# Optimization experiments

Hardware: AMD Instinct MI355X
Metric: run time of the kernel (lower is better)

Reference implementation:

```python
import jax, jax.numpy as jnp
import numpy as np

N_ITER = 5
EPS = 1e-20


def setup_inputs() -> dict:
    key = jax.random.key(0)
    k1, k2, k3 = jax.random.split(key, 3)
    M, J, I, K, N = 2, 2048, 2049, 8, 2
    X = jax.random.normal(k1, (M, J, I, 2), dtype=jnp.float32)
    # torch.rand(...) * (1 - 1e-8) + 1e-8  (hoisted out of forward for determinism)
    T0 = jax.random.uniform(k2, (I, K, N), dtype=jnp.float32) * (1 - 1e-8) + 1e-8
    V0 = jax.random.uniform(k3, (K, J, N), dtype=jnp.float32) * (1 - 1e-8) + 1e-8
    return {"X": X, "T0": T0, "V0": V0}


def _ilrma(X_ri, T0, V0):
    # X_ri: (M, J, I, 2) real -> Xc: (I, M, J) complex
    Xp = jnp.transpose(X_ri, (2, 0, 1, 3))
    Xc = jax.lax.complex(Xp[..., 0], Xp[..., 1])
    I_, M, J = Xc.shape
    N = T0.shape[2]
    W = jnp.broadcast_to(jnp.eye(N, M, dtype=Xc.dtype), (I_, N, M))  # (I, N, M)
    Y = jnp.einsum('inm,imj->inj', W, Xc)                            # (I, N, J)
    T, V = T0, V0
    invJ = jnp.asarray(1.0 / J, dtype=Xc.dtype)
    for _ in range(N_ITER):
        for n in range(N):
            Tn = T[:, :, n]            # (I, K)
            Vn = V[:, :, n]            # (K, J)
            Yn = Y[:, n, :]            # (I, J)
            # --- NMF multiplicative updates (vectorized over all I bins) ---
            Rn = Tn @ Vn                                        # (I, J)
            P = jnp.abs(Yn) ** 2 / (jnp.abs(Rn) ** 2 + EPS)     # |Y|^2 / R^2
            Rd = 1.0 / jnp.abs(Rn)                              # 1 / R
            Tn = Tn * jnp.sqrt((P @ Vn.T) / (Rd @ Vn.T))
            Rn = Tn @ Vn
            Vn = Vn * jnp.sqrt((Tn.T @ P) / (Tn.T @ Rd))
            Rn = Tn @ Vn                                        # updated source model
            T = T.at[:, :, n].set(Tn)
            V = V.at[:, :, n].set(Vn)
            # --- demixing vector update, batched over frequency bins I ---
            Xh = Xc / Rn[:, None, :]                            # (I, M, J)
            D = jnp.einsum('imj,ikj->imk', Xh, Xc) * invJ       # (I, M, M) (plain .T, no conj, as in source)
            WD = jnp.einsum('inm,imk->ink', W, D)               # (I, M, M)
            e = jnp.zeros((M,), dtype=Xc.dtype).at[n].set(1.0)
            rhs = jnp.broadcast_to(e[:, None], (I_, M, 1))
            b = jnp.linalg.solve(WD, rhs)[..., 0]               # (I, M)  == inv(W D) @ e_n
            nrm = jnp.einsum('im,imk,ik->i', b, D, b)           # b^T D b (complex, no conj)
            W = W.at[:, :, n].set(b / jnp.sqrt(nrm)[:, None])
        Y = jnp.einsum('inm,imj->inj', W, Xc)
    return Y


def reference(X, T0, V0):
    return _ilrma(X, T0, V0)
```

## Files before the change

### kernel.cpp

```cpp
#include <hip/hip_runtime.h>
#include <math.h>

#define I_  2049
#define M_  2
#define J_  2048
#define K_  8
#define N_  2
#define NITER 5
#define EPSF 1e-20f
#define INVJ (1.0/2048.0)
#define CHUNK 16
#define NCHUNK 129

__device__ float4 g_Xc[(size_t)I_*J_];
__device__ float2 g_T2[I_*K_];
__device__ float2 g_Told2[I_*K_];
__device__ float4 g_Vt4[(size_t)J_*4];
__device__ float2 g_W[I_*N_*M_];
__device__ float2 g_Wold[I_*N_*M_];
__device__ float2 g_pnum[(size_t)NCHUNK*K_*J_];
__device__ float2 g_pden[(size_t)NCHUNK*K_*J_];

__device__ __forceinline__ float frcp(float x) { return __builtin_amdgcn_rcpf(x); }

struct dcx { double x, y; };
__device__ __forceinline__ dcx cmul(dcx a, dcx b) { return {a.x*b.x - a.y*b.y, a.x*b.y + a.y*b.x}; }
__device__ __forceinline__ dcx cadd(dcx a, dcx b) { return {a.x + b.x, a.y + b.y}; }
__device__ __forceinline__ dcx csub(dcx a, dcx b) { return {a.x - b.x, a.y - b.y}; }
__device__ __forceinline__ dcx cneg(dcx a) { return {-a.x, -a.y}; }
__device__ __forceinline__ dcx cdiv(dcx a, dcx b) {
  double d = b.x*b.x + b.y*b.y;
  return {(a.x*b.x + a.y*b.y)/d, (a.y*b.x - a.x*b.y)/d};
}
__device__ __forceinline__ dcx csqrt_(dcx z) {
  double r = hypot(z.x, z.y);
  if (r == 0.0) return {0.0, 0.0};
  double t = sqrt(0.5*(r + fabs(z.x)));
  if (z.x >= 0.0) return {t, z.y/(2.0*t)};
  return {fabs(z.y)/(2.0*t), (z.y >= 0.0) ? t : -t};
}

__device__ __forceinline__ float2 cyn(float2 w0, float2 w1, float2 x0, float2 x1) {
  float2 y;
  y.x = w0.x*x0.x - w0.y*x0.y + w1.x*x1.x - w1.y*x1.y;
  y.y = w0.x*x0.y + w0.y*x0.x + w1.x*x1.y + w1.y*x1.x;
  return y;
}

__device__ __forceinline__ void solve12(int i, const double* s_, float2* wout) {
  dcx Wl[2][2];
  Wl[0][0] = {g_W[(size_t)i*4+0].x, g_W[(size_t)i*4+0].y};
  Wl[0][1] = {g_W[(size_t)i*4+1].x, g_W[(size_t)i*4+1].y};
  Wl[1][0] = {g_W[(size_t)i*4+2].x, g_W[(size_t)i*4+2].y};
  Wl[1][1] = {g_W[(size_t)i*4+3].x, g_W[(size_t)i*4+3].y};
#pragma unroll
  for (int n = 0; n < N_; n++) {
    dcx D00 = {s_[6*n+0]*INVJ, s_[6*n+1]*INVJ};
    dcx D01 = {s_[6*n+2]*INVJ, s_[6*n+3]*INVJ};
    dcx D11 = {s_[6*n+4]*INVJ, s_[6*n+5]*INVJ};
    dcx WD00 = cadd(cmul(Wl[0][0], D00), cmul(Wl[0][1], D01));
    dcx WD01 = cadd(cmul(Wl[0][0], D01), cmul(Wl[0][1], D11));
    dcx WD10 = cadd(cmul(Wl[1][0], D00), cmul(Wl[1][1], D01));
    dcx WD11 = cadd(cmul(Wl[1][0], D01), cmul(Wl[1][1], D11));
    dcx det = csub(cmul(WD00, WD11), cmul(WD01, WD10));
    dcx b0, b1;
    if (n == 0) { b0 = cdiv(WD11, det);        b1 = cdiv(cneg(WD10), det); }
    else        { b0 = cdiv(cneg(WD01), det);  b1 = cdiv(WD00, det); }
    dcx nrm = cadd(cmul(cmul(b0, b0), D00), cmul(cmul(b1, b1), D11));
    dcx tcr = cmul(cmul(b0, b1), D01); tcr.x *= 2.0; tcr.y *= 2.0;
    nrm = cadd(nrm, tcr);
    dcx sq = csqrt_(nrm);
    Wl[0][n] = cdiv(b0, sq);
    Wl[1][n] = cdiv(b1, sq);
  }
  float2 o00 = make_float2((float)Wl[0][0].x, (float)Wl[0][0].y);
  float2 o01 = make_float2((float)Wl[0][1].x, (float)Wl[0][1].y);
  float2 o10 = make_float2((float)Wl[1][0].x, (float)Wl[1][0].y);
  float2 o11 = make_float2((float)Wl[1][1].x, (float)Wl[1][1].y);
  g_W[(size_t)i*4+0] = o00; g_W[(size_t)i*4+1] = o01;
  g_W[(size_t)i*4+2] = o10; g_W[(size_t)i*4+3] = o11;
  g_Wold[(size_t)i*4+0] = o00; g_Wold[(size_t)i*4+1] = o01;
  g_Wold[(size_t)i*4+2] = o10; g_Wold[(size_t)i*4+3] = o11;
  wout[0] = o00; wout[1] = o01; wout[2] = o10; wout[3] = o11;
}

__global__ __launch_bounds__(256) void k_setup(const float* __restrict__ T0,
                                               const float* __restrict__ V0) {
  int idx = blockIdx.x*256 + threadIdx.x;
  if (idx < I_*K_) g_T2[idx] = ((const float2*)T0)[idx];
  if (idx < K_*J_) {
    int k = idx >> 11, j = idx & (J_-1);
    float2 v = ((const float2*)V0)[idx];
    float* vtf = (float*)g_Vt4;
    vtf[j*16 + k]     = v.x;
    vtf[j*16 + 8 + k] = v.y;
  }
  if (idx < I_*N_*M_) {
    int r = (idx >> 1) & 1, c = idx & 1;
    float2 v = make_float2((r == c) ? 1.f : 0.f, 0.f);
    g_W[idx] = v;
    g_Wold[idx] = v;
  }
}

__global__ __launch_bounds__(256) void k_transpose(const float* __restrict__ X) {
  __shared__ float2 s0[32][65];
  __shared__ float2 s1[32][65];
  int i0 = blockIdx.x*64, j0 = blockIdx.y*32;
  int lane = threadIdx.x & 63, row = threadIdx.x >> 6;
  const float2* X2 = (const float2*)X;
  int gi = i0 + lane;
  if (gi < I_) {
    for (int jj = row; jj < 32; jj += 4) {
      s0[jj][lane] = X2[(size_t)(0*J_ + j0 + jj)*I_ + gi];
      s1[jj][lane] = X2[(size_t)(1*J_ + j0 + jj)*I_ + gi];
    }
  }
  __syncthreads();
  int jj = threadIdx.x & 31, ii0 = threadIdx.x >> 5;
  for (int u = 0; u < 8; u++) {
    int ii = ii0*8 + u;
    int i = i0 + ii;
    if (i < I_) {
      float2 a = s0[jj][ii], b = s1[jj][ii];
      g_Xc[(size_t)i*J_ + j0 + jj] = make_float4(a.x, a.y, b.x, b.y);
    }
  }
}

__global__ __launch_bounds__(256) void k_tv(int doD) {
  int i = blockIdx.x, t = threadIdx.x;
  int wv = t >> 6, lane = t & 63;
  __shared__ float redD[4][12];
  __shared__ float2 sW[4];
  __shared__ float redT[4][32];

  float2 tk2[K_];
#pragma unroll
  for (int k = 0; k < K_; k++) tk2[k] = g_T2[(size_t)i*K_ + k];

  if (doD) {
    float4 xv[8];
#pragma unroll
    for (int s = 0; s < 8; s++) xv[s] = g_Xc[(size_t)i*J_ + wv*512 + s*64 + lane];
    float acc[12];
#pragma unroll
    for (int q = 0; q < 12; q++) acc[q] = 0.f;
#pragma unroll
    for (int s = 0; s < 8; s++) {
      int j = wv*512 + s*64 + lane;
      float4 vt0 = g_Vt4[(size_t)j*4+0], vt1 = g_Vt4[(size_t)j*4+1];
      float4 vt2 = g_Vt4[(size_t)j*4+2], vt3 = g_Vt4[(size_t)j*4+3];
      float vkx[K_] = {vt0.x,vt0.y,vt0.z,vt0.w,vt1.x,vt1.y,vt1.z,vt1.w};
      float vky[K_] = {vt2.x,vt2.y,vt2.z,vt2.w,vt3.x,vt3.y,vt3.z,vt3.w};
      float rn0 = 0.f, rn1 = 0.f;
#pragma unroll
      for (int k = 0; k < K_; k++) {
        rn0 = fmaf(tk2[k].x, vkx[k], rn0);
        rn1 = fmaf(tk2[k].y, vky[k], rn1);
      }
      float a0 = xv[s].x, b0 = xv[s].y, a1 = xv[s].z, b1 = xv[s].w;
      float d00r = a0*a0 - b0*b0, d00i = 2.f*a0*b0;
      float d01r = a0*a1 - b0*b1, d01i = a0*b1 + a1*b0;
      float d11r = a1*a1 - b1*b1, d11i = 2.f*a1*b1;
      float inv0 = frcp(rn0), inv1 = frcp(rn1);
      acc[0] = fmaf(d00r, inv0, acc[0]); acc[1] = fmaf(d00i, inv0, acc[1]);
      acc[2] = fmaf(d01r, inv0, acc[2]); acc[3] = fmaf(d01i, inv0, acc[3]);
      acc[4] = fmaf(d11r, inv0, acc[4]); acc[5] = fmaf(d11i, inv0, acc[5]);
      acc[6] = fmaf(d00r, inv1, acc[6]); acc[7] = fmaf(d00i, inv1, acc[7]);
      acc[8] = fmaf(d01r, inv1, acc[8]); acc[9] = fmaf(d01i, inv1, acc[9]);
      acc[10]= fmaf(d11r, inv1, acc[10]);acc[11]= fmaf(d11i, inv1, acc[11]);
    }
#pragma unroll
    for (int q = 0; q < 12; q++)
      for (int off = 32; off; off >>= 1) acc[q] += __shfl_down(acc[q], off);
    if (lane == 0) {
#pragma unroll
      for (int q = 0; q < 12; q++) redD[wv][q] = acc[q];
    }
    __syncthreads();
    if (t == 0) {
      double s_[12];
#pragma unroll
      for (int q = 0; q < 12; q++)
        s_[q] = (double)redD[0][q] + (double)redD[1][q] + (double)redD[2][q] + (double)redD[3][q];
      float2 w[4];
      solve12(i, s_, w);
      sW[0] = w[0]; sW[1] = w[1]; sW[2] = w[2]; sW[3] = w[3];
    }
  } else {
    if (t == 0) {
      sW[0] = g_Wold[(size_t)i*4+0]; sW[1] = g_Wold[(size_t)i*4+1];
      sW[2] = g_Wold[(size_t)i*4+2]; sW[3] = g_Wold[(size_t)i*4+3];
    }
  }
  __syncthreads();
  float2 w00 = sW[0], w01 = sW[1], w10 = sW[2], w11 = sW[3];

  float4 xv2[8];
#pragma unroll
  for (int s = 0; s < 8; s++) xv2[s] = g_Xc[(size_t)i*J_ + t + 256*s];
  float aN0[K_], aD0[K_], aN1[K_], aD1[K_];
#pragma unroll
  for (int k = 0; k < K_; k++) { aN0[k]=0.f; aD0[k]=0.f; aN1[k]=0.f; aD1[k]=0.f; }
#pragma unroll
  for (int s = 0; s < 8; s++) {
    int j = t + 256*s;
    float4 vt0 = g_Vt4[(size_t)j*4+0], vt1 = g_Vt4[(size_t)j*4+1];
    float4 vt2 = g_Vt4[(size_t)j*4+2], vt3 = g_Vt4[(size_t)j*4+3];
    float vkx[K_] = {vt0.x,vt0.y,vt0.z,vt0.w,vt1.x,vt1.y,vt1.z,vt1.w};
    float vky[K_] = {vt2.x,vt2.y,vt2.z,vt2.w,vt3.x,vt3.y,vt3.z,vt3.w};
    float rn0 = 0.f, rn1 = 0.f;
#pragma unroll
    for (int k = 0; k < K_; k++) {
      rn0 = fmaf(tk2[k].x, vkx[k], rn0);
      rn1 = fmaf(tk2[k].y, vky[k], rn1);
    }
    float2 x0 = make_float2(xv2[s].x, xv2[s].y);
    float2 x1 = make_float2(xv2[s].z, xv2[s].w);
    float2 y0 = cyn(w00, w01, x0, x1);
    float2 y1 = cyn(w10, w11, x0, x1);
    float p0  = (y0.x*y0.x + y0.y*y0.y) * frcp(rn0*rn0 + EPSF);
    float p1  = (y1.x*y1.x + y1.y*y1.y) * frcp(rn1*rn1 + EPSF);
    float rd0 = frcp(rn0), rd1 = frcp(rn1);
#pragma unroll
    for (int k = 0; k < K_; k++) {
      aN0[k] = fmaf(p0,  vkx[k], aN0[k]);
      aD0[k] = fmaf(rd0, vkx[k], aD0[k]);
      aN1[k] = fmaf(p1,  vky[k], aN1[k]);
      aD1[k] = fmaf(rd1, vky[k], aD1[k]);
    }
  }
#pragma unroll
  for (int k = 0; k < K_; k++)
    for (int off = 32; off; off >>= 1) {
      aN0[k] += __shfl_down(aN0[k], off);
      aD0[k] += __shfl_down(aD0[k], off);
      aN1[k] += __shfl_down(aN1[k], off);
      aD1[k] += __shfl_down(aD1[k], off);
    }
  if (lane == 0) {
#pragma unroll
    for (int k = 0; k < K_; k++) {
      redT[wv][k]      = aN0[k];
      redT[wv][8 + k]  = aD0[k];
      redT[wv][16 + k] = aN1[k];
      redT[wv][24 + k] = aD1[k];
    }
  }
  __syncthreads();
  if (t < 8) {
    int k = t;
    float n0 = redT[0][k]    + redT[1][k]    + redT[2][k]    + redT[3][k];
    float d0 = redT[0][8+k]  + redT[1][8+k]  + redT[2][8+k]  + redT[3][8+k];
    float n1 = redT[0][16+k] + redT[1][16+k] + redT[2][16+k] + redT[3][16+k];
    float d1 = redT[0][24+k] + redT[1][24+k] + redT[2][24+k] + redT[3][24+k];
    float2 tv = tk2[k];
    g_Told2[(size_t)i*K_ + k] = tv;
    g_T2[(size_t)i*K_ + k] = make_float2(tv.x * sqrtf(n0/d0), tv.y * sqrtf(n1/d1));
  }
}

__global__ __launch_bounds__(256) void k_vupd2() {
  int t  = threadIdx.x;
  int j  = blockIdx.x*256 + t;
  int c  = blockIdx.y;
  int i0 = c*CHUNK;
  int ni = I_ - i0; if (ni > CHUNK) ni = CHUNK;

  __shared__ float2 sWold[CHUNK*4];
  __shared__ float2 sTold[CHUNK*8];
  __shared__ float2 sT[CHUNK*8];
  for (int u = t; u < CHUNK*20; u += 256) {
    if (u < CHUNK*4) {
      int g = i0*4 + u;              if (g < I_*4) sWold[u] = g_Wold[g];
    } else if (u < CHUNK*12) {
      int g = i0*8 + (u - CHUNK*4);  if (g < I_*8) sTold[u - CHUNK*4] = g_Told2[g];
    } else {
      int g = i0*8 + (u - CHUNK*12); if (g < I_*8) sT[u - CHUNK*12] = g_T2[g];
    }
  }
  __syncthreads();

  float4 vt0 = g_Vt4[(size_t)j*4+0], vt1 = g_Vt4[(size_t)j*4+1];
  float4 vt2 = g_Vt4[(size_t)j*4+2], vt3 = g_Vt4[(size_t)j*4+3];
  float vkx[K_] = {vt0.x,vt0.y,vt0.z,vt0.w,vt1.x,vt1.y,vt1.z,vt1.w};
  float vky[K_] = {vt2.x,vt2.y,vt2.z,vt2.w,vt3.x,vt3.y,vt3.z,vt3.w};
  float aN0[K_], aD0[K_], aN1[K_], aD1[K_];
#pragma unroll
  for (int k = 0; k < K_; k++) { aN0[k]=0.f; aD0[k]=0.f; aN1[k]=0.f; aD1[k]=0.f; }

  auto body = [&](int ii, float4 xv) {
    float2 x0 = make_float2(xv.x, xv.y);
    float2 x1 = make_float2(xv.z, xv.w);
    float2 w00 = sWold[ii*4 + 0], w01 = sWold[ii*4 + 1];
    float2 w10 = sWold[ii*4 + 2], w11 = sWold[ii*4 + 3];
    float rn0 = 0.f, rn1 = 0.f;
#pragma unroll
    for (int k = 0; k < K_; k++) {
      float2 to = sTold[ii*8 + k];
      rn0 = fmaf(to.x, vkx[k], rn0);
      rn1 = fmaf(to.y, vky[k], rn1);
    }
    float2 y0 = cyn(w00, w01, x0, x1);
    float2 y1 = cyn(w10, w11, x0, x1);
    float p0  = (y0.x*y0.x + y0.y*y0.y) * frcp(rn0*rn0 + EPSF);
    float p1  = (y1.x*y1.x + y1.y*y1.y) * frcp(rn1*rn1 + EPSF);
    float rd0 = frcp(rn0), rd1 = frcp(rn1);
#pragma unroll
    for (int k = 0; k < K_; k++) {
      float2 tn = sT[ii*8 + k];
      aN0[k] = fmaf(tn.x, p0,  aN0[k]);
      aD0[k] = fmaf(tn.x, rd0, aD0[k]);
      aN1[k] = fmaf(tn.y, p1,  aN1[k]);
      aD1[k] = fmaf(tn.y, rd1, aD1[k]);
    }
  };

  int ii = 0;
  for (; ii + 8 <= ni; ii += 8) {
    float4 xv[8];
#pragma unroll
    for (int u = 0; u < 8; u++) xv[u] = g_Xc[(size_t)(i0 + ii + u)*J_ + j];
#pragma unroll
    for (int u = 0; u < 8; u++) body(ii + u, xv[u]);
  }
  for (; ii < ni; ii++) {
    float4 xv = g_Xc[(size_t)(i0 + ii)*J_ + j];
    body(ii, xv);
  }

  size_t base = (size_t)c*(K_*J_);
#pragma unroll
  for (int k = 0; k < K_; k++) {
    g_pnum[base + (size_t)k*J_ + j] = make_float2(aN0[k], aN1[k]);
    g_pden[base + (size_t)k*J_ + j] = make_float2(aD0[k], aD1[k]);
  }
}

__global__ __launch_bounds__(256) void k_vapply2() {
  int t = threadIdx.x;
  int idx = blockIdx.x*16 + (t & 15);
  int slice = t >> 4;
  int c0 = slice*9, c1 = c0 + 9; if (c1 > NCHUNK) c1 = NCHUNK;
  float2 sn = make_float2(0.f, 0.f), sd = make_float2(0.f, 0.f);
  for (int c = c0; c < c1; c++) {
    float2 a = g_pnum[(size_t)c*(K_*J_) + idx];
    float2 b = g_pden[(size_t)c*(K_*J_) + idx];
    sn.x += a.x; sn.y += a.y; sd.x += b.x; sd.y += b.y;
  }
  __shared__ float2 rN[16][16], rD[16][16];
  rN[slice][t & 15] = sn; rD[slice][t & 15] = sd;
  __syncthreads();
  if (t < 16) {
    float2 n = rN[0][t], d = rD[0][t];
#pragma unroll
    for (int s = 1; s < 16; s++) {
      n.x += rN[s][t].x; n.y += rN[s][t].y;
      d.x += rD[s][t].x; d.y += rD[s][t].y;
    }
    int kk = idx >> 11, j = idx & (J_-1);
    float* vtf = (float*)g_Vt4;
    float v0 = vtf[j*16 + kk], v1 = vtf[j*16 + 8 + kk];
    vtf[j*16 + kk]     = v0 * sqrtf(n.x/d.x);
    vtf[j*16 + 8 + kk] = v1 * sqrtf(n.y/d.y);
  }
}

__global__ __launch_bounds__(256) void k_yout(float* __restrict__ out, int cplx) {
  int i = blockIdx.x, t = threadIdx.x;
  int wv = t >> 6, lane = t & 63;
  __shared__ float redD[4][12];
  __shared__ float2 sW[4];

  float2 tk2[K_];
#pragma unroll
  for (int k = 0; k < K_; k++) tk2[k] = g_T2[(size_t)i*K_ + k];

  {
    float4 xv[8];
#pragma unroll
    for (int s = 0; s < 8; s++) xv[s] = g_Xc[(size_t)i*J_ + wv*512 + s*64 + lane];
    float acc[12];
#pragma unroll
    for (int q = 0; q < 12; q++) acc[q] = 0.f;
#pragma unroll
    for (int s = 0; s < 8; s++) {
      int j = wv*512 + s*64 + lane;
      float4 vt0 = g_Vt4[(size_t)j*4+0], vt1 = g_Vt4[(size_t)j*4+1];
      float4 vt2 = g_Vt4[(size_t)j*4+2], vt3 = g_Vt4[(size_t)j*4+3];
      float vkx[K_] = {vt0.x,vt0.y,vt0.z,vt0.w,vt1.x,vt1.y,vt1.z,vt1.w};
      float vky[K_] = {vt2.x,vt2.y,vt2.z,vt2.w,vt3.x,vt3.y,vt3.z,vt3.w};
      float rn0 = 0.f, rn1 = 0.f;
#pragma unroll
      for (int k = 0; k < K_; k++) {
        rn0 = fmaf(tk2[k].x, vkx[k], rn0);
        rn1 = fmaf(tk2[k].y, vky[k], rn1);
      }
      float a0 = xv[s].x, b0 = xv[s].y, a1 = xv[s].z, b1 = xv[s].w;
      float d00r = a0*a0 - b0*b0, d00i = 2.f*a0*b0;
      float d01r = a0*a1 - b0*b1, d01i = a0*b1 + a1*b0;
      float d11r = a1*a1 - b1*b1, d11i = 2.f*a1*b1;
      float inv0 = frcp(rn0), inv1 = frcp(rn1);
      acc[0] = fmaf(d00r, inv0, acc[0]); acc[1] = fmaf(d00i, inv0, acc[1]);
      acc[2] = fmaf(d01r, inv0, acc[2]); acc[3] = fmaf(d01i, inv0, acc[3]);
      acc[4] = fmaf(d11r, inv0, acc[4]); acc[5] = fmaf(d11i, inv0, acc[5]);
      acc[6] = fmaf(d00r, inv1, acc[6]); acc[7] = fmaf(d00i, inv1, acc[7]);
      acc[8] = fmaf(d01r, inv1, acc[8]); acc[9] = fmaf(d01i, inv1, acc[9]);
      acc[10]= fmaf(d11r, inv1, acc[10]);acc[11]= fmaf(d11i, inv1, acc[11]);
    }
#pragma unroll
    for (int q = 0; q < 12; q++)
      for (int off = 32; off; off >>= 1) acc[q] += __shfl_down(acc[q], off);
    if (lane == 0) {
#pragma unroll
      for (int q = 0; q < 12; q++) redD[wv][q] = acc[q];
    }
  }
  __syncthreads();
  if (t == 0) {
    double s_[12];
#pragma unroll
    for (int q = 0; q < 12; q++)
      s_[q] = (double)redD[0][q] + (double)redD[1][q] + (double)redD[2][q] + (double)redD[3][q];
    float2 w[4];
    solve12(i, s_, w);
    sW[0] = w[0]; sW[1] = w[1]; sW[2] = w[2]; sW[3] = w[3];
  }
  __syncthreads();
  float2 w00 = sW[0], w01 = sW[1], w10 = sW[2], w11 = sW[3];
  float2* out2 = (float2*)out;
#pragma unroll
  for (int s = 0; s < 8; s++) {
    int j = t + 256*s;
    float4 xv = g_Xc[(size_t)i*J_ + j];
    float2 x0 = make_float2(xv.x, xv.y);
    float2 x1 = make_float2(xv.z, xv.w);
    float2 y0 = cyn(w00, w01, x0, x1);
    float2 y1 = cyn(w10, w11, x0, x1);
    if (cplx) {
      out2[((size_t)i*N_ + 0)*J_ + j] = y0;
      out2[((size_t)i*N_ + 1)*J_ + j] = y1;
    } else {
      out[((size_t)i*N_ + 0)*J_ + j] = y0.x;
      out[((size_t)i*N_ + 1)*J_ + j] = y1.x;
    }
  }
}

extern "C" void kernel_launch(void* const* d_in, const int* in_sizes, int n_in,
                              void* d_out, int out_size, void* d_ws, size_t ws_size,
                              hipStream_t stream) {
  const float* X  = (const float*)d_in[0];
  const float* T0 = (const float*)d_in[1];
  const float* V0 = (const float*)d_in[2];
  (void)d_ws; (void)ws_size;

  k_setup<<<(I_*K_ + 255)/256, 256, 0, stream>>>(T0, V0);
  k_transpose<<<dim3((I_ + 63)/64, J_/32), 256, 0, stream>>>(X);

  int cplx = (out_size >= 2*I_*N_*J_) ? 1 : 0;
  for (int it = 0; it < NITER; it++) {
    k_tv<<<I_, 256, 0, stream>>>(it > 0);
    k_vupd2<<<dim3(J_/256, NCHUNK), 256, 0, stream>>>();
    k_vapply2<<<K_*J_/16, 256, 0, stream>>>();
  }
  k_yout<<<I_, 256, 0, stream>>>((float*)d_out, cplx);
}
```

Before: 611.6 us.

## Store T in transposed float4 layout and vectorize partial-sum buffers

T moves from interleaved float2 per k to a planar layout of 16 floats per bin, so each block loads it as four float4 and dot products use vectorized float4 math. The V-update partial sums move from float2 per k into four float4 arrays grouped by k, so k_vapply2 reduces four k values per thread with float4 loads and launches a quarter as many blocks. Launch bounds of 256 threads with a minimum of 2 blocks are added to the main kernels. The aim is fewer, wider memory transactions and less scalar load and address overhead; the launch-bound hint also caps register use, which could cause spills.

```diff
diff --git a/kernel.cpp b/kernel.cpp
--- a/kernel.cpp
+++ b/kernel.cpp
@@ -2,7 +2,6 @@
 #include <math.h>
 
 #define I_  2049
-#define M_  2
 #define J_  2048
 #define K_  8
 #define N_  2
@@ -13,15 +12,40 @@
 #define NCHUNK 129
 
 __device__ float4 g_Xc[(size_t)I_*J_];
-__device__ float2 g_T2[I_*K_];
-__device__ float2 g_Told2[I_*K_];
+__device__ float  g_Tt[I_*16];
+__device__ float  g_Toldt[I_*16];
 __device__ float4 g_Vt4[(size_t)J_*4];
-__device__ float2 g_W[I_*N_*M_];
-__device__ float2 g_Wold[I_*N_*M_];
-__device__ float2 g_pnum[(size_t)NCHUNK*K_*J_];
-__device__ float2 g_pden[(size_t)NCHUNK*K_*J_];
+__device__ float2 g_W[I_*4];
+__device__ float2 g_Wold[I_*4];
+__device__ float4 g_pnA[(size_t)NCHUNK*2*J_];
+__device__ float4 g_pnB[(size_t)NCHUNK*2*J_];
+__device__ float4 g_pdA[(size_t)NCHUNK*2*J_];
+__device__ float4 g_pdB[(size_t)NCHUNK*2*J_];
 
 __device__ __forceinline__ float frcp(float x) { return __builtin_amdgcn_rcpf(x); }
+
+__device__ __forceinline__ float dot44(float4 a, float4 b) {
+  return fmaf(a.x, b.x, fmaf(a.y, b.y, fmaf(a.z, b.z, a.w*b.w)));
+}
+__device__ __forceinline__ float4 f4fma(float s, float4 v, float4 a) {
+  a.x = fmaf(s, v.x, a.x); a.y = fmaf(s, v.y, a.y);
+  a.z = fmaf(s, v.z, a.z); a.w = fmaf(s, v.w, a.w);
+  return a;
+}
+__device__ __forceinline__ float4 f4add(float4 a, float4 b) {
+  return make_float4(a.x+b.x, a.y+b.y, a.z+b.z, a.w+b.w);
+}
+__device__ __forceinline__ float4 wred4(float4 v) {
+  v.x += __shfl_down(v.x,32); v.y += __shfl_down(v.y,32); v.z += __shfl_down(v.z,32); v.w += __shfl_down(v.w,32);
+  v.x += __shfl_down(v.x,16); v.y += __shfl_down(v.y,16); v.z += __shfl_down(v.z,16); v.w += __shfl_down(v.w,16);
+  v.x += __shfl_down(v.x, 8); v.y += __shfl_down(v.y, 8); v.z += __shfl_down(v.z, 8); v.w += __shfl_down(v.w, 8);
+  v.x += __shfl_down(v.x, 4); v.y += __shfl_down(v.y, 4); v.z += __shfl_down(v.z, 4); v.w += __shfl_down(v.w, 4);
+  v.x += __shfl_down(v.x, 2); v.y += __shfl_down(v.y, 2); v.z += __shfl_down(v.z, 2); v.w += __shfl_down(v.w, 2);
+  v.x += __shfl_down(v.x, 1); v.y += __shfl_down(v.y, 1); v.z += __shfl_down(v.z, 1); v.w += __shfl_down(v.w, 1);
+  return v;
+}
+#define RW(x) { x += __shfl_down(x,32); x += __shfl_down(x,16); x += __shfl_down(x,8); \
+                x += __shfl_down(x,4);  x += __shfl_down(x,2);  x += __shfl_down(x,1); }
 
 struct dcx { double x, y; };
 __device__ __forceinline__ dcx cmul(dcx a, dcx b) { return {a.x*b.x - a.y*b.y, a.x*b.y + a.y*b.x}; }
@@ -87,7 +111,12 @@
 __global__ __launch_bounds__(256) void k_setup(const float* __restrict__ T0,
                                                const float* __restrict__ V0) {
   int idx = blockIdx.x*256 + threadIdx.x;
-  if (idx < I_*K_) g_T2[idx] = ((const float2*)T0)[idx];
+  if (idx < I_*K_) {
+    int i = idx >> 3, k = idx & 7;
+    float2 v = ((const float2*)T0)[idx];
+    g_Tt[i*16 + k]     = v.x;
+    g_Tt[i*16 + 8 + k] = v.y;
+  }
   if (idx < K_*J_) {
     int k = idx >> 11, j = idx & (J_-1);
     float2 v = ((const float2*)V0)[idx];
@@ -95,7 +124,7 @@
     vtf[j*16 + k]     = v.x;
     vtf[j*16 + 8 + k] = v.y;
   }
-  if (idx < I_*N_*M_) {
+  if (idx < I_*4) {
     int r = (idx >> 1) & 1, c = idx & 1;
     float2 v = make_float2((r == c) ? 1.f : 0.f, 0.f);
     g_W[idx] = v;
@@ -128,55 +157,45 @@
   }
 }
 
-__global__ __launch_bounds__(256) void k_tv(int doD) {
+__global__ __launch_bounds__(256, 2) void k_tv(int doD) {
   int i = blockIdx.x, t = threadIdx.x;
   int wv = t >> 6, lane = t & 63;
   __shared__ float redD[4][12];
   __shared__ float2 sW[4];
   __shared__ float redT[4][32];
 
-  float2 tk2[K_];
-#pragma unroll
-  for (int k = 0; k < K_; k++) tk2[k] = g_T2[(size_t)i*K_ + k];
+  const float4* T4 = (const float4*)g_Tt;
+  float4 tt0 = T4[i*4+0], tt1 = T4[i*4+1];
+  float4 tt2 = T4[i*4+2], tt3 = T4[i*4+3];
 
   if (doD) {
-    float4 xv[8];
-#pragma unroll
-    for (int s = 0; s < 8; s++) xv[s] = g_Xc[(size_t)i*J_ + wv*512 + s*64 + lane];
-    float acc[12];
-#pragma unroll
-    for (int q = 0; q < 12; q++) acc[q] = 0.f;
-#pragma unroll
-    for (int s = 0; s < 8; s++) {
-      int j = wv*512 + s*64 + lane;
-      float4 vt0 = g_Vt4[(size_t)j*4+0], vt1 = g_Vt4[(size_t)j*4+1];
-      float4 vt2 = g_Vt4[(size_t)j*4+2], vt3 = g_Vt4[(size_t)j*4+3];
-      float vkx[K_] = {vt0.x,vt0.y,vt0.z,vt0.w,vt1.x,vt1.y,vt1.z,vt1.w};
-      float vky[K_] = {vt2.x,vt2.y,vt2.z,vt2.w,vt3.x,vt3.y,vt3.z,vt3.w};
-      float rn0 = 0.f, rn1 = 0.f;
-#pragma unroll
-      for (int k = 0; k < K_; k++) {
-        rn0 = fmaf(tk2[k].x, vkx[k], rn0);
-        rn1 = fmaf(tk2[k].y, vky[k], rn1);
-      }
-      float a0 = xv[s].x, b0 = xv[s].y, a1 = xv[s].z, b1 = xv[s].w;
-      float d00r = a0*a0 - b0*b0, d00i = 2.f*a0*b0;
-      float d01r = a0*a1 - b0*b1, d01i = a0*b1 + a1*b0;
-      float d11r = a1*a1 - b1*b1, d11i = 2.f*a1*b1;
-      float inv0 = frcp(rn0), inv1 = frcp(rn1);
-      acc[0] = fmaf(d00r, inv0, acc[0]); acc[1] = fmaf(d00i, inv0, acc[1]);
-      acc[2] = fmaf(d01r, inv0, acc[2]); acc[3] = fmaf(d01i, inv0, acc[3]);
-      acc[4] = fmaf(d11r, inv0, acc[4]); acc[5] = fmaf(d11i, inv0, acc[5]);
-      acc[6] = fmaf(d00r, inv1, acc[6]); acc[7] = fmaf(d00i, inv1, acc[7]);
-      acc[8] = fmaf(d01r, inv1, acc[8]); acc[9] = fmaf(d01i, inv1, acc[9]);
-      acc[10]= fmaf(d11r, inv1, acc[10]);acc[11]= fmaf(d11i, inv1, acc[11]);
-    }
-#pragma unroll
-    for (int q = 0; q < 12; q++)
-      for (int off = 32; off; off >>= 1) acc[q] += __shfl_down(acc[q], off);
+    size_t xb = (size_t)i*J_ + wv*512 + lane;
+    float4 xv0 = g_Xc[xb+0*64], xv1 = g_Xc[xb+1*64], xv2 = g_Xc[xb+2*64], xv3 = g_Xc[xb+3*64];
+    float4 xv4 = g_Xc[xb+4*64], xv5 = g_Xc[xb+5*64], xv6 = g_Xc[xb+6*64], xv7 = g_Xc[xb+7*64];
+    float s0=0.f,s1=0.f,s2=0.f,s3=0.f,s4=0.f,s5=0.f,s6=0.f,s7=0.f,s8=0.f,s9=0.f,s10=0.f,s11=0.f;
+#define DB(U) { int j = wv*512 + U*64 + lane; \
+    const float4* Vp = g_Vt4 + (size_t)j*4; \
+    float4 vt0=Vp[0], vt1=Vp[1], vt2=Vp[2], vt3=Vp[3]; \
+    float rn0 = dot44(tt0,vt0)+dot44(tt1,vt1); \
+    float rn1 = dot44(tt2,vt2)+dot44(tt3,vt3); \
+    float a0=xv##U.x, b0=xv##U.y, a1=xv##U.z, b1=xv##U.w; \
+    float e00r=a0*a0-b0*b0, e00i=2.f*a0*b0; \
+    float e01r=a0*a1-b0*b1, e01i=a0*b1+a1*b0; \
+    float e11r=a1*a1-b1*b1, e11i=2.f*a1*b1; \
+    float inv0=frcp(rn0), inv1=frcp(rn1); \
+    s0=fmaf(e00r,inv0,s0);  s1=fmaf(e00i,inv0,s1); \
+    s2=fmaf(e01r,inv0,s2);  s3=fmaf(e01i,inv0,s3); \
+    s4=fmaf(e11r,inv0,s4);  s5=fmaf(e11i,inv0,s5); \
+    s6=fmaf(e00r,inv1,s6);  s7=fmaf(e00i,inv1,s7); \
+    s8=fmaf(e01r,inv1,s8);  s9=fmaf(e01i,inv1,s9); \
+    s10=fmaf(e11r,inv1,s10); s11=fmaf(e11i,inv1,s11); }
+    DB(0) DB(1) DB(2) DB(3) DB(4) DB(5) DB(6) DB(7)
+#undef DB
+    RW(s0) RW(s1) RW(s2) RW(s3) RW(s4) RW(s5) RW(s6) RW(s7) RW(s8) RW(s9) RW(s10) RW(s11)
     if (lane == 0) {
-#pragma unroll
-      for (int q = 0; q < 12; q++) redD[wv][q] = acc[q];
+      redD[wv][0]=s0;  redD[wv][1]=s1;  redD[wv][2]=s2;  redD[wv][3]=s3;
+      redD[wv][4]=s4;  redD[wv][5]=s5;  redD[wv][6]=s6;  redD[wv][7]=s7;
+      redD[wv][8]=s8;  redD[wv][9]=s9;  redD[wv][10]=s10; redD[wv][11]=s11;
     }
     __syncthreads();
     if (t == 0) {
@@ -197,56 +216,38 @@
   __syncthreads();
   float2 w00 = sW[0], w01 = sW[1], w10 = sW[2], w11 = sW[3];
 
-  float4 xv2[8];
-#pragma unroll
-  for (int s = 0; s < 8; s++) xv2[s] = g_Xc[(size_t)i*J_ + t + 256*s];
-  float aN0[K_], aD0[K_], aN1[K_], aD1[K_];
-#pragma unroll
-  for (int k = 0; k < K_; k++) { aN0[k]=0.f; aD0[k]=0.f; aN1[k]=0.f; aD1[k]=0.f; }
-#pragma unroll
-  for (int s = 0; s < 8; s++) {
-    int j = t + 256*s;
-    float4 vt0 = g_Vt4[(size_t)j*4+0], vt1 = g_Vt4[(size_t)j*4+1];
-    float4 vt2 = g_Vt4[(size_t)j*4+2], vt3 = g_Vt4[(size_t)j*4+3];
-    float vkx[K_] = {vt0.x,vt0.y,vt0.z,vt0.w,vt1.x,vt1.y,vt1.z,vt1.w};
-    float vky[K_] = {vt2.x,vt2.y,vt2.z,vt2.w,vt3.x,vt3.y,vt3.z,vt3.w};
-    float rn0 = 0.f, rn1 = 0.f;
-#pragma unroll
-    for (int k = 0; k < K_; k++) {
-      rn0 = fmaf(tk2[k].x, vkx[k], rn0);
-      rn1 = fmaf(tk2[k].y, vky[k], rn1);
-    }
-    float2 x0 = make_float2(xv2[s].x, xv2[s].y);
-    float2 x1 = make_float2(xv2[s].z, xv2[s].w);
-    float2 y0 = cyn(w00, w01, x0, x1);
-    float2 y1 = cyn(w10, w11, x0, x1);
-    float p0  = (y0.x*y0.x + y0.y*y0.y) * frcp(rn0*rn0 + EPSF);
-    float p1  = (y1.x*y1.x + y1.y*y1.y) * frcp(rn1*rn1 + EPSF);
-    float rd0 = frcp(rn0), rd1 = frcp(rn1);
-#pragma unroll
-    for (int k = 0; k < K_; k++) {
-      aN0[k] = fmaf(p0,  vkx[k], aN0[k]);
-      aD0[k] = fmaf(rd0, vkx[k], aD0[k]);
-      aN1[k] = fmaf(p1,  vky[k], aN1[k]);
-      aD1[k] = fmaf(rd1, vky[k], aD1[k]);
-    }
-  }
-#pragma unroll
-  for (int k = 0; k < K_; k++)
-    for (int off = 32; off; off >>= 1) {
-      aN0[k] += __shfl_down(aN0[k], off);
-      aD0[k] += __shfl_down(aD0[k], off);
-      aN1[k] += __shfl_down(aN1[k], off);
-      aD1[k] += __shfl_down(aD1[k], off);
-    }
+  size_t yb = (size_t)i*J_ + t;
+  float4 xw0 = g_Xc[yb+0*256], xw1 = g_Xc[yb+1*256], xw2 = g_Xc[yb+2*256], xw3 = g_Xc[yb+3*256];
+  float4 xw4 = g_Xc[yb+4*256], xw5 = g_Xc[yb+5*256], xw6 = g_Xc[yb+6*256], xw7 = g_Xc[yb+7*256];
+  float4 z = make_float4(0.f,0.f,0.f,0.f);
+  float4 aN0a=z, aN0b=z, aD0a=z, aD0b=z, aN1a=z, aN1b=z, aD1a=z, aD1b=z;
+#define TB(U) { int j = t + U*256; \
+  const float4* Vp = g_Vt4 + (size_t)j*4; \
+  float4 vt0=Vp[0], vt1=Vp[1], vt2=Vp[2], vt3=Vp[3]; \
+  float rn0 = dot44(tt0,vt0)+dot44(tt1,vt1); \
+  float rn1 = dot44(tt2,vt2)+dot44(tt3,vt3); \
+  float2 x0=make_float2(xw##U.x,xw##U.y), x1=make_float2(xw##U.z,xw##U.w); \
+  float2 y0=cyn(w00,w01,x0,x1), y1=cyn(w10,w11,x0,x1); \
+  float p0=(y0.x*y0.x+y0.y*y0.y)*frcp(rn0*rn0+EPSF); \
+  float p1=(y1.x*y1.x+y1.y*y1.y)*frcp(rn1*rn1+EPSF); \
+  float rd0=frcp(rn0), rd1=frcp(rn1); \
+  aN0a=f4fma(p0,vt0,aN0a); aN0b=f4fma(p0,vt1,aN0b); \
+  aD0a=f4fma(rd0,vt0,aD0a); aD0b=f4fma(rd0,vt1,aD0b); \
+  aN1a=f4fma(p1,vt2,aN1a); aN1b=f4fma(p1,vt3,aN1b); \
+  aD1a=f4fma(rd1,vt2,aD1a); aD1b=f4fma(rd1,vt3,aD1b); }
+  TB(0) TB(1) TB(2) TB(3) TB(4) TB(5) TB(6) TB(7)
+#undef TB
+  aN0a = wred4(aN0a); aN0b = wred4(aN0b); aD0a = wred4(aD0a); aD0b = wred4(aD0b);
+  aN1a = wred4(aN1a); aN1b = wred4(aN1b); aD1a = wred4(aD1a); aD1b = wred4(aD1b);
   if (lane == 0) {
-#pragma unroll
-    for (int k = 0; k < K_; k++) {
-      redT[wv][k]      = aN0[k];
-      redT[wv][8 + k]  = aD0[k];
-      redT[wv][16 + k] = aN1[k];
-      redT[wv][24 + k] = aD1[k];
-    }
+    redT[wv][0]=aN0a.x;  redT[wv][1]=aN0a.y;  redT[wv][2]=aN0a.z;  redT[wv][3]=aN0a.w;
+    redT[wv][4]=aN0b.x;  redT[wv][5]=aN0b.y;  redT[wv][6]=aN0b.z;  redT[wv][7]=aN0b.w;
+    redT[wv][8]=aD0a.x;  redT[wv][9]=aD0a.y;  redT[wv][10]=aD0a.z; redT[wv][11]=aD0a.w;
+    redT[wv][12]=aD0b.x; redT[wv][13]=aD0b.y; redT[wv][14]=aD0b.z; redT[wv][15]=aD0b.w;
+    redT[wv][16]=aN1a.x; redT[wv][17]=aN1a.y; redT[wv][18]=aN1a.z; redT[wv][19]=aN1a.w;
+    redT[wv][20]=aN1b.x; redT[wv][21]=aN1b.y; redT[wv][22]=aN1b.z; redT[wv][23]=aN1b.w;
+    redT[wv][24]=aD1a.x; redT[wv][25]=aD1a.y; redT[wv][26]=aD1a.z; redT[wv][27]=aD1a.w;
+    redT[wv][28]=aD1b.x; redT[wv][29]=aD1b.y; redT[wv][30]=aD1b.z; redT[wv][31]=aD1b.w;
   }
   __syncthreads();
   if (t < 8) {
@@ -255,13 +256,15 @@
     float d0 = redT[0][8+k]  + redT[1][8+k]  + redT[2][8+k]  + redT[3][8+k];
     float n1 = redT[0][16+k] + redT[1][16+k] + redT[2][16+k] + redT[3][16+k];
     float d1 = redT[0][24+k] + redT[1][24+k] + redT[2][24+k] + redT[3][24+k];
-    float2 tv = tk2[k];
-    g_Told2[(size_t)i*K_ + k] = tv;
-    g_T2[(size_t)i*K_ + k] = make_float2(tv.x * sqrtf(n0/d0), tv.y * sqrtf(n1/d1));
-  }
-}
-
-__global__ __launch_bounds__(256) void k_vupd2() {
+    float tvx = g_Tt[i*16 + k], tvy = g_Tt[i*16 + 8 + k];
+    g_Toldt[i*16 + k]     = tvx;
+    g_Toldt[i*16 + 8 + k] = tvy;
+    g_Tt[i*16 + k]     = tvx * sqrtf(n0/d0);
+    g_Tt[i*16 + 8 + k] = tvy * sqrtf(n1/d1);
+  }
+}
+
+__global__ __launch_bounds__(256, 2) void k_vupd2() {
   int t  = threadIdx.x;
   int j  = blockIdx.x*256 + t;
   int c  = blockIdx.y;
@@ -269,152 +272,135 @@
   int ni = I_ - i0; if (ni > CHUNK) ni = CHUNK;
 
   __shared__ float2 sWold[CHUNK*4];
-  __shared__ float2 sTold[CHUNK*8];
-  __shared__ float2 sT[CHUNK*8];
-  for (int u = t; u < CHUNK*20; u += 256) {
-    if (u < CHUNK*4) {
-      int g = i0*4 + u;              if (g < I_*4) sWold[u] = g_Wold[g];
-    } else if (u < CHUNK*12) {
-      int g = i0*8 + (u - CHUNK*4);  if (g < I_*8) sTold[u - CHUNK*4] = g_Told2[g];
-    } else {
-      int g = i0*8 + (u - CHUNK*12); if (g < I_*8) sT[u - CHUNK*12] = g_T2[g];
-    }
-  }
-  __syncthreads();
-
-  float4 vt0 = g_Vt4[(size_t)j*4+0], vt1 = g_Vt4[(size_t)j*4+1];
-  float4 vt2 = g_Vt4[(size_t)j*4+2], vt3 = g_Vt4[(size_t)j*4+3];
-  float vkx[K_] = {vt0.x,vt0.y,vt0.z,vt0.w,vt1.x,vt1.y,vt1.z,vt1.w};
-  float vky[K_] = {vt2.x,vt2.y,vt2.z,vt2.w,vt3.x,vt3.y,vt3.z,vt3.w};
-  float aN0[K_], aD0[K_], aN1[K_], aD1[K_];
-#pragma unroll
-  for (int k = 0; k < K_; k++) { aN0[k]=0.f; aD0[k]=0.f; aN1[k]=0.f; aD1[k]=0.f; }
+  __shared__ float4 sTold[CHUNK*4];
+  __shared__ float4 sT[CHUNK*4];
+  const float4* To4 = (const float4*)g_Toldt;
+  const float4* Tn4 = (const float4*)g_Tt;
+  if (t < CHUNK*4) {
+    int g = i0*4 + t; if (g < I_*4) sWold[t] = g_Wold[g];
+  } else if (t < CHUNK*8) {
+    int u = t - CHUNK*4; int g = i0*4 + u; if (g < I_*4) sTold[u] = To4[g];
+  } else if (t < CHUNK*12) {
+    int u = t - CHUNK*8; int g = i0*4 + u; if (g < I_*4) sT[u] = Tn4[g];
+  }
+  __syncthreads();
+
+  const float4* Vp = g_Vt4 + (size_t)j*4;
+  float4 vt0 = Vp[0], vt1 = Vp[1], vt2 = Vp[2], vt3 = Vp[3];
+  float4 z = make_float4(0.f,0.f,0.f,0.f);
+  float4 aN0a=z, aN0b=z, aD0a=z, aD0b=z, aN1a=z, aN1b=z, aD1a=z, aD1b=z;
 
   auto body = [&](int ii, float4 xv) {
-    float2 x0 = make_float2(xv.x, xv.y);
-    float2 x1 = make_float2(xv.z, xv.w);
-    float2 w00 = sWold[ii*4 + 0], w01 = sWold[ii*4 + 1];
-    float2 w10 = sWold[ii*4 + 2], w11 = sWold[ii*4 + 3];
-    float rn0 = 0.f, rn1 = 0.f;
-#pragma unroll
-    for (int k = 0; k < K_; k++) {
-      float2 to = sTold[ii*8 + k];
-      rn0 = fmaf(to.x, vkx[k], rn0);
-      rn1 = fmaf(to.y, vky[k], rn1);
-    }
-    float2 y0 = cyn(w00, w01, x0, x1);
-    float2 y1 = cyn(w10, w11, x0, x1);
-    float p0  = (y0.x*y0.x + y0.y*y0.y) * frcp(rn0*rn0 + EPSF);
-    float p1  = (y1.x*y1.x + y1.y*y1.y) * frcp(rn1*rn1 + EPSF);
+    float2 x0 = make_float2(xv.x, xv.y), x1 = make_float2(xv.z, xv.w);
+    float2 w00 = sWold[ii*4+0], w01 = sWold[ii*4+1], w10 = sWold[ii*4+2], w11 = sWold[ii*4+3];
+    float4 to0 = sTold[ii*4+0], to1 = sTold[ii*4+1], to2 = sTold[ii*4+2], to3 = sTold[ii*4+3];
+    float rn0 = dot44(to0,vt0)+dot44(to1,vt1);
+    float rn1 = dot44(to2,vt2)+dot44(to3,vt3);
+    float2 y0 = cyn(w00,w01,x0,x1), y1 = cyn(w10,w11,x0,x1);
+    float p0 = (y0.x*y0.x+y0.y*y0.y)*frcp(rn0*rn0+EPSF);
+    float p1 = (y1.x*y1.x+y1.y*y1.y)*frcp(rn1*rn1+EPSF);
     float rd0 = frcp(rn0), rd1 = frcp(rn1);
-#pragma unroll
-    for (int k = 0; k < K_; k++) {
-      float2 tn = sT[ii*8 + k];
-      aN0[k] = fmaf(tn.x, p0,  aN0[k]);
-      aD0[k] = fmaf(tn.x, rd0, aD0[k]);
-      aN1[k] = fmaf(tn.y, p1,  aN1[k]);
-      aD1[k] = fmaf(tn.y, rd1, aD1[k]);
-    }
+    float4 st0 = sT[ii*4+0], st1 = sT[ii*4+1], st2 = sT[ii*4+2], st3 = sT[ii*4+3];
+    aN0a = f4fma(p0,  st0, aN0a); aN0b = f4fma(p0,  st1, aN0b);
+    aD0a = f4fma(rd0, st0, aD0a); aD0b = f4fma(rd0, st1, aD0b);
+    aN1a = f4fma(p1,  st2, aN1a); aN1b = f4fma(p1,  st3, aN1b);
+    aD1a = f4fma(rd1, st2, aD1a); aD1b = f4fma(rd1, st3, aD1b);
   };
 
   int ii = 0;
   for (; ii + 8 <= ni; ii += 8) {
-    float4 xv[8];
-#pragma unroll
-    for (int u = 0; u < 8; u++) xv[u] = g_Xc[(size_t)(i0 + ii + u)*J_ + j];
-#pragma unroll
-    for (int u = 0; u < 8; u++) body(ii + u, xv[u]);
-  }
-  for (; ii < ni; ii++) {
-    float4 xv = g_Xc[(size_t)(i0 + ii)*J_ + j];
-    body(ii, xv);
-  }
-
-  size_t base = (size_t)c*(K_*J_);
-#pragma unroll
-  for (int k = 0; k < K_; k++) {
-    g_pnum[base + (size_t)k*J_ + j] = make_float2(aN0[k], aN1[k]);
-    g_pden[base + (size_t)k*J_ + j] = make_float2(aD0[k], aD1[k]);
-  }
+    float4 xA = g_Xc[(size_t)(i0+ii+0)*J_ + j];
+    float4 xB = g_Xc[(size_t)(i0+ii+1)*J_ + j];
+    float4 xC = g_Xc[(size_t)(i0+ii+2)*J_ + j];
+    float4 xD = g_Xc[(size_t)(i0+ii+3)*J_ + j];
+    float4 xE = g_Xc[(size_t)(i0+ii+4)*J_ + j];
+    float4 xF = g_Xc[(size_t)(i0+ii+5)*J_ + j];
+    float4 xG = g_Xc[(size_t)(i0+ii+6)*J_ + j];
+    float4 xH = g_Xc[(size_t)(i0+ii+7)*J_ + j];
+    body(ii+0,xA); body(ii+1,xB); body(ii+2,xC); body(ii+3,xD);
+    body(ii+4,xE); body(ii+5,xF); body(ii+6,xG); body(ii+7,xH);
+  }
+  for (; ii < ni; ii++) body(ii, g_Xc[(size_t)(i0+ii)*J_ + j]);
+
+  size_t b2 = (size_t)c*2*J_;
+  g_pnA[b2 + j] = aN0a;  g_pnA[b2 + J_ + j] = aN0b;
+  g_pnB[b2 + j] = aN1a;  g_pnB[b2 + J_ + j] = aN1b;
+  g_pdA[b2 + j] = aD0a;  g_pdA[b2 + J_ + j] = aD0b;
+  g_pdB[b2 + j] = aD1a;  g_pdB[b2 + J_ + j] = aD1b;
 }
 
 __global__ __launch_bounds__(256) void k_vapply2() {
   int t = threadIdx.x;
-  int idx = blockIdx.x*16 + (t & 15);
+  int g = blockIdx.x*16 + (t & 15);
   int slice = t >> 4;
+  int kg = g >> 11, j = g & (J_-1);
   int c0 = slice*9, c1 = c0 + 9; if (c1 > NCHUNK) c1 = NCHUNK;
-  float2 sn = make_float2(0.f, 0.f), sd = make_float2(0.f, 0.f);
+  float4 z = make_float4(0.f,0.f,0.f,0.f);
+  float4 sNa=z, sNb=z, sDa=z, sDb=z;
   for (int c = c0; c < c1; c++) {
-    float2 a = g_pnum[(size_t)c*(K_*J_) + idx];
-    float2 b = g_pden[(size_t)c*(K_*J_) + idx];
-    sn.x += a.x; sn.y += a.y; sd.x += b.x; sd.y += b.y;
-  }
-  __shared__ float2 rN[16][16], rD[16][16];
-  rN[slice][t & 15] = sn; rD[slice][t & 15] = sd;
+    size_t o = (size_t)c*2*J_ + (size_t)kg*J_ + j;
+    sNa = f4add(sNa, g_pnA[o]); sNb = f4add(sNb, g_pnB[o]);
+    sDa = f4add(sDa, g_pdA[o]); sDb = f4add(sDb, g_pdB[o]);
+  }
+  __shared__ float4 rNa[16][16], rNb[16][16], rDa[16][16], rDb[16][16];
+  rNa[slice][t & 15] = sNa; rNb[slice][t & 15] = sNb;
+  rDa[slice][t & 15] = sDa; rDb[slice][t & 15] = sDb;
   __syncthreads();
   if (t < 16) {
-    float2 n = rN[0][t], d = rD[0][t];
+    float4 na = rNa[0][t], nb = rNb[0][t], da = rDa[0][t], db = rDb[0][t];
 #pragma unroll
     for (int s = 1; s < 16; s++) {
-      n.x += rN[s][t].x; n.y += rN[s][t].y;
-      d.x += rD[s][t].x; d.y += rD[s][t].y;
-    }
-    int kk = idx >> 11, j = idx & (J_-1);
-    float* vtf = (float*)g_Vt4;
-    float v0 = vtf[j*16 + kk], v1 = vtf[j*16 + 8 + kk];
-    vtf[j*16 + kk]     = v0 * sqrtf(n.x/d.x);
-    vtf[j*16 + 8 + kk] = v1 * sqrtf(n.y/d.y);
-  }
-}
-
-__global__ __launch_bounds__(256) void k_yout(float* __restrict__ out, int cplx) {
+      na = f4add(na, rNa[s][t]); nb = f4add(nb, rNb[s][t]);
+      da = f4add(da, rDa[s][t]); db = f4add(db, rDb[s][t]);
+    }
+    int gg = blockIdx.x*16 + t;
+    int kg2 = gg >> 11, j2 = gg & (J_-1);
+    float4 v0 = g_Vt4[(size_t)j2*4 + kg2];
+    float4 v1 = g_Vt4[(size_t)j2*4 + 2 + kg2];
+    v0.x *= sqrtf(na.x/da.x); v0.y *= sqrtf(na.y/da.y); v0.z *= sqrtf(na.z/da.z); v0.w *= sqrtf(na.w/da.w);
+    v1.x *= sqrtf(nb.x/db.x); v1.y *= sqrtf(nb.y/db.y); v1.z *= sqrtf(nb.z/db.z); v1.w *= sqrtf(nb.w/db.w);
+    g_Vt4[(size_t)j2*4 + kg2] = v0;
+    g_Vt4[(size_t)j2*4 + 2 + kg2] = v1;
+  }
+}
+
+__global__ __launch_bounds__(256, 2) void k_yout(float* __restrict__ out, int cplx) {
   int i = blockIdx.x, t = threadIdx.x;
   int wv = t >> 6, lane = t & 63;
   __shared__ float redD[4][12];
   __shared__ float2 sW[4];
 
-  float2 tk2[K_];
-#pragma unroll
-  for (int k = 0; k < K_; k++) tk2[k] = g_T2[(size_t)i*K_ + k];
+  const float4* T4 = (const float4*)g_Tt;
+  float4 tt0 = T4[i*4+0], tt1 = T4[i*4+1], tt2 = T4[i*4+2], tt3 = T4[i*4+3];
 
   {
-    float4 xv[8];
-#pragma unroll
-    for (int s = 0; s < 8; s++) xv[s] = g_Xc[(size_t)i*J_ + wv*512 + s*64 + lane];
-    float acc[12];
-#pragma unroll
-    for (int q = 0; q < 12; q++) acc[q] = 0.f;
-#pragma unroll
-    for (int s = 0; s < 8; s++) {
-      int j = wv*512 + s*64 + lane;
-      float4 vt0 = g_Vt4[(size_t)j*4+0], vt1 = g_Vt4[(size_t)j*4+1];
-      float4 vt2 = g_Vt4[(size_t)j*4+2], vt3 = g_Vt4[(size_t)j*4+3];
-      float vkx[K_] = {vt0.x,vt0.y,vt0.z,vt0.w,vt1.x,vt1.y,vt1.z,vt1.w};
-      float vky[K_] = {vt2.x,vt2.y,vt2.z,vt2.w,vt3.x,vt3.y,vt3.z,vt3.w};
-      float rn0 = 0.f, rn1 = 0.f;
-#pragma unroll
-      for (int k = 0; k < K_; k++) {
-        rn0 = fmaf(tk2[k].x, vkx[k], rn0);
-        rn1 = fmaf(tk2[k].y, vky[k], rn1);
-      }
-      float a0 = xv[s].x, b0 = xv[s].y, a1 = xv[s].z, b1 = xv[s].w;
-      float d00r = a0*a0 - b0*b0, d00i = 2.f*a0*b0;
-      float d01r = a0*a1 - b0*b1, d01i = a0*b1 + a1*b0;
-      float d11r = a1*a1 - b1*b1, d11i = 2.f*a1*b1;
-      float inv0 = frcp(rn0), inv1 = frcp(rn1);
-      acc[0] = fmaf(d00r, inv0, acc[0]); acc[1] = fmaf(d00i, inv0, acc[1]);
-      acc[2] = fmaf(d01r, inv0, acc[2]); acc[3] = fmaf(d01i, inv0, acc[3]);
-      acc[4] = fmaf(d11r, inv0, acc[4]); acc[5] = fmaf(d11i, inv0, acc[5]);
-      acc[6] = fmaf(d00r, inv1, acc[6]); acc[7] = fmaf(d00i, inv1, acc[7]);
-      acc[8] = fmaf(d01r, inv1, acc[8]); acc[9] = fmaf(d01i, inv1, acc[9]);
-      acc[10]= fmaf(d11r, inv1, acc[10]);acc[11]= fmaf(d11i, inv1, acc[11]);
-    }
-#pragma unroll
-    for (int q = 0; q < 12; q++)
-      for (int off = 32; off; off >>= 1) acc[q] += __shfl_down(acc[q], off);
+    size_t xb = (size_t)i*J_ + wv*512 + lane;
+    float4 xv0 = g_Xc[xb+0*64], xv1 = g_Xc[xb+1*64], xv2 = g_Xc[xb+2*64], xv3 = g_Xc[xb+3*64];
+    float4 xv4 = g_Xc[xb+4*64], xv5 = g_Xc[xb+5*64], xv6 = g_Xc[xb+6*64], xv7 = g_Xc[xb+7*64];
+    float s0=0.f,s1=0.f,s2=0.f,s3=0.f,s4=0.f,s5=0.f,s6=0.f,s7=0.f,s8=0.f,s9=0.f,s10=0.f,s11=0.f;
+#define DB(U) { int j = wv*512 + U*64 + lane; \
+    const float4* Vp = g_Vt4 + (size_t)j*4; \
+    float4 vt0=Vp[0], vt1=Vp[1], vt2=Vp[2], vt3=Vp[3]; \
+    float rn0 = dot44(tt0,vt0)+dot44(tt1,vt1); \
+    float rn1 = dot44(tt2,vt2)+dot44(tt3,vt3); \
+    float a0=xv##U.x, b0=xv##U.y, a1=xv##U.z, b1=xv##U.w; \
+    float e00r=a0*a0-b0*b0, e00i=2.f*a0*b0; \
+    float e01r=a0*a1-b0*b1, e01i=a0*b1+a1*b0; \
+    float e11r=a1*a1-b1*b1, e11i=2.f*a1*b1; \
+    float inv0=frcp(rn0), inv1=frcp(rn1); \
+    s0=fmaf(e00r,inv0,s0);  s1=fmaf(e00i,inv0,s1); \
+    s2=fmaf(e01r,inv0,s2);  s3=fmaf(e01i,inv0,s3); \
+    s4=fmaf(e11r,inv0,s4);  s5=fmaf(e11i,inv0,s5); \
+    s6=fmaf(e00r,inv1,s6);  s7=fmaf(e00i,inv1,s7); \
+    s8=fmaf(e01r,inv1,s8);  s9=fmaf(e01i,inv1,s9); \
+    s10=fmaf(e11r,inv1,s10); s11=fmaf(e11i,inv1,s11); }
+    DB(0) DB(1) DB(2) DB(3) DB(4) DB(5) DB(6) DB(7)
+#undef DB
+    RW(s0) RW(s1) RW(s2) RW(s3) RW(s4) RW(s5) RW(s6) RW(s7) RW(s8) RW(s9) RW(s10) RW(s11)
     if (lane == 0) {
-#pragma unroll
-      for (int q = 0; q < 12; q++) redD[wv][q] = acc[q];
+      redD[wv][0]=s0;  redD[wv][1]=s1;  redD[wv][2]=s2;  redD[wv][3]=s3;
+      redD[wv][4]=s4;  redD[wv][5]=s5;  redD[wv][6]=s6;  redD[wv][7]=s7;
+      redD[wv][8]=s8;  redD[wv][9]=s9;  redD[wv][10]=s10; redD[wv][11]=s11;
     }
   }
   __syncthreads();
@@ -463,7 +449,7 @@
   for (int it = 0; it < NITER; it++) {
     k_tv<<<I_, 256, 0, stream>>>(it > 0);
     k_vupd2<<<dim3(J_/256, NCHUNK), 256, 0, stream>>>();
-    k_vapply2<<<K_*J_/16, 256, 0, stream>>>();
+    k_vapply2<<<2*J_/16, 256, 0, stream>>>();
   }
   k_yout<<<I_, 256, 0, stream>>>((float*)d_out, cplx);
 }
```

Measured after the change: 542.9 us. 1.13x faster.
